# Performance work log

Measured on AMD Instinct MI355X. Metric: run time of the kernel, lower is better.

## Reference

```python
import jax, jax.numpy as jnp
import numpy as np

B, L, N, IN, OUT = 32, 512, 128, 16, 10
BN_EPS = 1e-5


def setup_inputs() -> dict:
    key = jax.random.key(0)
    ks = jax.random.split(key, 10)
    def lin(k, fan_in, fan_out):
        bound = 1.0 / np.sqrt(fan_in)
        return jax.random.uniform(k, (fan_in, fan_out), jnp.float32, -bound, bound)
    x = jax.random.normal(ks[0], (B, L, IN), jnp.float32)
    # binary tree adjacency mask (n_nodes, n_leaves), ~0/1 entries
    tree = jax.random.randint(ks[1], (N, L), 0, 2).astype(jnp.float32)
    return {
        "x": x, "tree": tree,
        "W1": lin(ks[2], IN, 32), "b1": jnp.zeros((32,), jnp.float32),
        "W2": lin(ks[3], 32, 64), "b2": jnp.zeros((64,), jnp.float32),
        "W3": lin(ks[4], 64, 16), "b3": jnp.zeros((16,), jnp.float32),
        "W4": lin(ks[5], N * 16, 64), "b4": jnp.zeros((64,), jnp.float32),
        "gamma": jnp.ones((64,), jnp.float32), "beta": jnp.zeros((64,), jnp.float32),
        "W5": lin(ks[6], 64, OUT), "b5": jnp.zeros((OUT,), jnp.float32),
    }


def reference(x, tree, W1, b1, W2, b2, W3, b3, W4, b4, gamma, beta, W5, b5):
    # f_micro: (B, L, IN) -> (B, L, 64)
    h = jax.nn.relu(x @ W1 + b1)
    h = jax.nn.relu(h @ W2 + b2)
    # masked multiply + max over leaves for every tree node, vectorized:
    # h_agg[b, n, c] = max_l h[b, l, c] * tree[n, l]   -> (B, N, 64)
    h_agg = jnp.max(h[:, None, :, :] * tree[None, :, :, None], axis=2)
    # f_macro + flatten: (B, N, 16) -> (B, N*16)
    m = jax.nn.relu(h_agg @ W3 + b3).reshape(h_agg.shape[0], -1)
    # f_out: Linear -> ReLU -> BatchNorm1d (training mode, batch stats) -> Linear
    y = jax.nn.relu(m @ W4 + b4)
    mean = jnp.mean(y, axis=0)
    var = jnp.mean(jnp.square(y - mean), axis=0)  # biased variance, as torch BN
    yn = (y - mean) * jax.lax.rsqrt(var + BN_EPS) * gamma + beta
    return yn @ W5 + b5
```

## Files before the change

### kernel.cpp

```cpp
#include <hip/hip_runtime.h>
#include <hip/hip_fp16.h>


static __device__ __forceinline__ unsigned pk_max_f16(unsigned a, unsigned b) {
    unsigned r;
    asm("v_pk_max_f16 %0, %1, %2" : "=v"(r) : "v"(a), "v"(b));
    return r;
}

__global__ __launch_bounds__(256) void k_micro(
    const float* __restrict__ x, const float* __restrict__ W1,
    const float* __restrict__ b1, const float* __restrict__ W2,
    const float* __restrict__ b2, unsigned* __restrict__ h16,
    unsigned long long* __restrict__ yfix)
{
    const int gid = blockIdx.x;
    const int xcd = gid & 7;
    const int t   = gid >> 3;
    const int bq  = t >> 4;
    const int rb  = t & 15;
    const int b   = bq * 8 + xcd;
    const int row0 = b * 512 + rb * 32;

    const int tid = threadIdx.x;
    const int r = tid >> 5;
    const int p = tid & 31;

    if (gid == 0) {
        for (int i = tid; i < 2048; i += 256) yfix[i] = 0ull;
    }

    __shared__ float sx[32][16];
    __shared__ float sh1[32][32];

    {
        float v0 = x[(size_t)row0 * 16 + tid];
        float v1 = x[(size_t)row0 * 16 + 256 + tid];
        ((float*)sx)[tid]       = v0;
        ((float*)sx)[tid + 256] = v1;
    }

    float w1c[16];
    #pragma unroll
    for (int i = 0; i < 16; ++i) w1c[i] = W1[i * 32 + p];
    float2 w2[32];
    #pragma unroll
    for (int j = 0; j < 32; ++j) w2[j] = *(const float2*)&W2[j * 64 + 2 * p];
    const float  b1c = b1[p];
    const float2 b2p = *(const float2*)&b2[2 * p];
    __syncthreads();

    #pragma unroll
    for (int q = 0; q < 4; ++q) {
        const int row = q * 8 + r;
        float a = b1c;
        #pragma unroll
        for (int i = 0; i < 16; ++i) a += sx[row][i] * w1c[i];
        sh1[row][p] = fmaxf(a, 0.f);
    }
    __syncthreads();

    #pragma unroll
    for (int q = 0; q < 4; ++q) {
        const int row = q * 8 + r;
        float a0 = b2p.x, a1 = b2p.y;
        #pragma unroll
        for (int j = 0; j < 32; ++j) {
            const float v = sh1[row][j];
            a0 += v * w2[j].x;
            a1 += v * w2[j].y;
        }
        __half2 hp = __floats2half2_rn(fmaxf(a0, 0.f), fmaxf(a1, 0.f));
        h16[(size_t)(row0 + row) * 32 + p] = *(unsigned*)&hp;
    }
}

__global__ __launch_bounds__(512, 4) void k_agg_part(
    const unsigned* __restrict__ h16,
    const float* __restrict__ tree,
    const float* __restrict__ W3, const float* __restrict__ b3,
    const float* __restrict__ W4,
    unsigned long long* __restrict__ yfix)
{
    const int id   = blockIdx.x;
    const int xcd  = id & 7;
    const int ng   = (id >> 3) & 15;
    const int bq   = id >> 7;
    const int b    = bq * 8 + xcd;
    const int tid  = threadIdx.x;
    const int w    = tid >> 6;
    const int lane = tid & 63;
    const int g2   = lane >> 4;
    const int p2   = lane & 15;

    __shared__ unsigned smask[512];
    __shared__ float sred[8][8][64];
    __shared__ float sagg[8][64];
    __shared__ float sm[128];
    __shared__ float spart[8][64];

    {
        unsigned bits = 0;
        const float* tp = tree + (size_t)(ng * 8) * 512 + tid;
        #pragma unroll
        for (int n = 0; n < 8; ++n)
            if (tp[(size_t)n * 512] > 0.5f) bits |= (1u << n);
        smask[tid] = bits;
    }
    __syncthreads();

    unsigned accL[8], accH[8];
    #pragma unroll
    for (int n = 0; n < 8; ++n) { accL[n] = 0u; accH[n] = 0u; }

    const uint2* hb = (const uint2*)(h16 + (size_t)b * 16384
                                     + (size_t)(w * 64 + g2) * 32 + 2 * p2);
    const unsigned* mp = &smask[w * 64 + g2];
    #pragma unroll 16
    for (int j = 0; j < 16; ++j) {
        const uint2 hv = hb[(size_t)j * 64];
        const unsigned mb = mp[4 * j];
        #pragma unroll
        for (int n = 0; n < 8; ++n) {
            const int sel = (int)(mb << (31 - n)) >> 31;
            accL[n] = pk_max_f16(accL[n], hv.x & (unsigned)sel);
            accH[n] = pk_max_f16(accH[n], hv.y & (unsigned)sel);
        }
    }
    #pragma unroll
    for (int n = 0; n < 8; ++n) {
        accL[n] = pk_max_f16(accL[n], (unsigned)__shfl_xor((int)accL[n], 16));
        accH[n] = pk_max_f16(accH[n], (unsigned)__shfl_xor((int)accH[n], 16));
        accL[n] = pk_max_f16(accL[n], (unsigned)__shfl_xor((int)accL[n], 32));
        accH[n] = pk_max_f16(accH[n], (unsigned)__shfl_xor((int)accH[n], 32));
    }
    if (g2 == 0) {
        #pragma unroll
        for (int n = 0; n < 8; ++n) {
            const __half2 lo = *(const __half2*)&accL[n];
            const __half2 hi = *(const __half2*)&accH[n];
            *(float2*)&sred[w][n][4 * p2] =
                make_float2(__low2float(lo), __high2float(lo));
            *(float2*)&sred[w][n][4 * p2 + 2] =
                make_float2(__low2float(hi), __high2float(hi));
        }
    }
    __syncthreads();

    {
        const int n = tid >> 6, c = tid & 63;
        float v = sred[0][n][c];
        #pragma unroll
        for (int ww = 1; ww < 8; ++ww) v = fmaxf(v, sred[ww][n][c]);
        sagg[n][c] = v;
    }
    __syncthreads();

    if (tid < 128) {
        const int n = tid >> 4, jj = tid & 15;
        float a = b3[jj];
        #pragma unroll
        for (int c2 = 0; c2 < 64; ++c2)
            a += sagg[n][c2] * W3[c2 * 16 + jj];
        sm[tid] = fmaxf(a, 0.f);
    }
    __syncthreads();

    {
        float a = 0.f;
        const float* w4p = W4 + (size_t)(ng * 128 + w * 16) * 64 + lane;
        #pragma unroll
        for (int k2 = 0; k2 < 16; ++k2)
            a += sm[w * 16 + k2] * w4p[(size_t)k2 * 64];
        spart[w][lane] = a;
    }
    __syncthreads();
    if (tid < 64) {
        float v = 0.f;
        #pragma unroll
        for (int ww = 0; ww < 8; ++ww) v += spart[ww][tid];
        const long long q = llrintf(v * 4294967296.0f);
        atomicAdd(&yfix[(size_t)b * 64 + tid], (unsigned long long)q);
    }
}

__global__ __launch_bounds__(1024) void k_bn_out(
    const unsigned long long* __restrict__ yfix, const float* __restrict__ b4,
    const float* __restrict__ gamma, const float* __restrict__ beta,
    const float* __restrict__ W5, const float* __restrict__ b5,
    float* __restrict__ out)
{
    const int tid = threadIdx.x;
    __shared__ float sy[32 * 64];
    __shared__ float smean[64], sscale[64], sbeta[64];

    #pragma unroll
    for (int idx = tid; idx < 2048; idx += 1024) {
        const long long v = (long long)yfix[idx];
        sy[idx] = fmaxf((float)v * (1.0f / 4294967296.0f) + b4[idx & 63], 0.f);
    }
    __syncthreads();
    if (tid < 64) {
        float s1 = 0.f, s2 = 0.f;
        #pragma unroll
        for (int b = 0; b < 32; ++b) {
            const float v = sy[b * 64 + tid];
            s1 += v; s2 += v * v;
        }
        const float mean = s1 * (1.f / 32.f);
        const float var  = s2 * (1.f / 32.f) - mean * mean;
        smean[tid]  = mean;
        sscale[tid] = gamma[tid] * rsqrtf(var + 1e-5f);
        sbeta[tid]  = beta[tid];
    }
    __syncthreads();
    if (tid < 320) {
        const int b = tid / 10, q = tid % 10;
        float acc = b5[q];
        #pragma unroll
        for (int o = 0; o < 64; ++o)
            acc += ((sy[b * 64 + o] - smean[o]) * sscale[o] + sbeta[o])
                   * W5[o * 10 + q];
        out[b * 10 + q] = acc;
    }
}

extern "C" void kernel_launch(void* const* d_in, const int* in_sizes, int n_in,
                              void* d_out, int out_size, void* d_ws, size_t ws_size,
                              hipStream_t stream) {
    const float* x     = (const float*)d_in[0];
    const float* tree  = (const float*)d_in[1];
    const float* W1    = (const float*)d_in[2];
    const float* b1    = (const float*)d_in[3];
    const float* W2    = (const float*)d_in[4];
    const float* b2    = (const float*)d_in[5];
    const float* W3    = (const float*)d_in[6];
    const float* b3    = (const float*)d_in[7];
    const float* W4    = (const float*)d_in[8];
    const float* b4    = (const float*)d_in[9];
    const float* gamma = (const float*)d_in[10];
    const float* beta  = (const float*)d_in[11];
    const float* W5    = (const float*)d_in[12];
    const float* b5    = (const float*)d_in[13];
    float* out = (float*)d_out;

    unsigned*           h16  = (unsigned*)d_ws;
    unsigned long long* yfix = (unsigned long long*)(h16 + 16384 * 32);

    k_micro   <<<512,  256, 0, stream>>>(x, W1, b1, W2, b2, h16, yfix);
    k_agg_part<<<512,  512, 0, stream>>>(h16, tree, W3, b3, W4, yfix);
    k_bn_out  <<<1,   1024, 0, stream>>>(yfix, b4, gamma, beta, W5, b5, out);
}
```

Measured before the change: 22.99 us.

## Precompute tree bitmask table in micro kernel and halve its grid

```diff
diff --git a/kernel.cpp b/kernel.cpp
--- a/kernel.cpp
+++ b/kernel.cpp
@@ -9,35 +9,44 @@
 }
 
 __global__ __launch_bounds__(256) void k_micro(
-    const float* __restrict__ x, const float* __restrict__ W1,
-    const float* __restrict__ b1, const float* __restrict__ W2,
-    const float* __restrict__ b2, unsigned* __restrict__ h16,
+    const float* __restrict__ x, const float* __restrict__ tree,
+    const float* __restrict__ W1, const float* __restrict__ b1,
+    const float* __restrict__ W2, const float* __restrict__ b2,
+    unsigned* __restrict__ h16, unsigned* __restrict__ mask_tab,
     unsigned long long* __restrict__ yfix)
 {
     const int gid = blockIdx.x;
     const int xcd = gid & 7;
     const int t   = gid >> 3;
-    const int bq  = t >> 4;
-    const int rb  = t & 15;
+    const int bq  = t >> 3;
+    const int rb  = t & 7;
     const int b   = bq * 8 + xcd;
-    const int row0 = b * 512 + rb * 32;
+    const int row0 = b * 512 + rb * 64;
 
     const int tid = threadIdx.x;
     const int r = tid >> 5;
     const int p = tid & 31;
 
     if (gid == 0) {
+        #pragma unroll
         for (int i = tid; i < 2048; i += 256) yfix[i] = 0ull;
     }
 
-    __shared__ float sx[32][16];
-    __shared__ float sh1[32][32];
+    __shared__ float sx[64][16];
+    __shared__ float sh1[64][32];
+
+    #pragma unroll
+    for (int i = 0; i < 4; ++i)
+        ((float*)sx)[tid + 256 * i] = x[(size_t)row0 * 16 + tid + 256 * i];
 
     {
-        float v0 = x[(size_t)row0 * 16 + tid];
-        float v1 = x[(size_t)row0 * 16 + 256 + tid];
-        ((float*)sx)[tid]       = v0;
-        ((float*)sx)[tid + 256] = v1;
+        const int wv  = tid >> 6, l = tid & 63;
+        const int idx = gid * 8 + wv * 2 + (l >> 5);
+        const int w   = idx >> 9, leaf = idx & 511;
+        const bool pred = tree[(size_t)(w * 32 + (l & 31)) * 512 + leaf] > 0.5f;
+        const unsigned long long m = __ballot(pred);
+        if ((l & 31) == 0)
+            mask_tab[idx] = (unsigned)(m >> ((l >> 5) * 32));
     }
 
     float w1c[16];
@@ -51,7 +60,7 @@
     __syncthreads();
 
     #pragma unroll
-    for (int q = 0; q < 4; ++q) {
+    for (int q = 0; q < 8; ++q) {
         const int row = q * 8 + r;
         float a = b1c;
         #pragma unroll
@@ -61,7 +70,7 @@
     __syncthreads();
 
     #pragma unroll
-    for (int q = 0; q < 4; ++q) {
+    for (int q = 0; q < 8; ++q) {
         const int row = q * 8 + r;
         float a0 = b2p.x, a1 = b2p.y;
         #pragma unroll
@@ -77,7 +86,7 @@
 
 __global__ __launch_bounds__(512, 4) void k_agg_part(
     const unsigned* __restrict__ h16,
-    const float* __restrict__ tree,
+    const unsigned* __restrict__ mask_tab,
     const float* __restrict__ W3, const float* __restrict__ b3,
     const float* __restrict__ W4,
     unsigned long long* __restrict__ yfix)
@@ -99,14 +108,7 @@
     __shared__ float sm[128];
     __shared__ float spart[8][64];
 
-    {
-        unsigned bits = 0;
-        const float* tp = tree + (size_t)(ng * 8) * 512 + tid;
-        #pragma unroll
-        for (int n = 0; n < 8; ++n)
-            if (tp[(size_t)n * 512] > 0.5f) bits |= (1u << n);
-        smask[tid] = bits;
-    }
+    smask[tid] = (mask_tab[(ng >> 2) * 512 + tid] >> ((ng & 3) * 8)) & 0xffu;
     __syncthreads();
 
     unsigned accL[8], accH[8];
@@ -244,10 +246,12 @@
     const float* b5    = (const float*)d_in[13];
     float* out = (float*)d_out;
 
-    unsigned*           h16  = (unsigned*)d_ws;
-    unsigned long long* yfix = (unsigned long long*)(h16 + 16384 * 32);
-
-    k_micro   <<<512,  256, 0, stream>>>(x, W1, b1, W2, b2, h16, yfix);
-    k_agg_part<<<512,  512, 0, stream>>>(h16, tree, W3, b3, W4, yfix);
+    unsigned*           h16      = (unsigned*)d_ws;
+    unsigned long long* yfix     = (unsigned long long*)(h16 + 16384 * 32);
+    unsigned*           mask_tab = (unsigned*)(yfix + 2048);
+
+    k_micro   <<<256,  256, 0, stream>>>(x, tree, W1, b1, W2, b2,
+                                         h16, mask_tab, yfix);
+    k_agg_part<<<512,  512, 0, stream>>>(h16, mask_tab, W3, b3, W4, yfix);
     k_bn_out  <<<1,   1024, 0, stream>>>(yfix, b4, gamma, beta, W5, b5, out);
 }
```

After: 23.05 us. Within noise of the previous version (+0.3%).
